# Performance work log

Hardware: AMD Instinct MI355X
Metric: run time of the kernel (lower is better)

The kernel has to match this reference:

```python
import jax, jax.numpy as jnp
import numpy as np

B, S = 1, 2048
D = 4096          # hidden_size
H, HK, DH = 32, 8, 128  # num_heads, num_kv_heads, head_dim
THETA = 10000.0


def setup_inputs() -> dict:
    key = jax.random.key(0)
    k0, k1, k2, k3, k4 = jax.random.split(key, 5)
    std = 0.02
    return {
        "position_ids": jnp.broadcast_to(jnp.arange(S, dtype=jnp.int32), (B, S)),
        "hidden_states": jax.random.normal(k0, (B, S, D), jnp.float32),
        "Wq": (jax.random.normal(k1, (D, H * DH), jnp.float32) * std),
        "Wk": (jax.random.normal(k2, (D, HK * DH), jnp.float32) * std),
        "Wv": (jax.random.normal(k3, (D, HK * DH), jnp.float32) * std),
        "Wo": (jax.random.normal(k4, (H * DH, D), jnp.float32) * std),
    }


def _rope(x, pos):
    """Neox-style rotary embedding over the full head_dim. x: [B,S,h,DH]."""
    half = DH // 2
    inv_freq = 1.0 / (THETA ** (jnp.arange(half, dtype=jnp.float32) * 2.0 / DH))
    ang = pos[..., None].astype(jnp.float32) * inv_freq          # [B,S,half]
    cos = jnp.cos(ang)[:, :, None, :]
    sin = jnp.sin(ang)[:, :, None, :]
    x1, x2 = x[..., :half], x[..., half:]
    return jnp.concatenate([x1 * cos - x2 * sin, x2 * cos + x1 * sin], axis=-1)


def reference(position_ids, hidden_states, Wq, Wk, Wv, Wo):
    q = (hidden_states @ Wq).reshape(B, S, H, DH)
    k = (hidden_states @ Wk).reshape(B, S, HK, DH)
    v = (hidden_states @ Wv).reshape(B, S, HK, DH)
    q = _rope(q, position_ids)
    k = _rope(k, position_ids)

    G = H // HK  # query heads per kv head (GQA)
    qg = q.reshape(B, S, HK, G, DH)
    scale = jnp.float32(DH) ** -0.5
    scores = jnp.einsum('bqhgd,bkhd->bhgqk', qg, k) * scale      # [B,HK,G,S,S]
    causal = jnp.tril(jnp.ones((S, S), dtype=bool))
    scores = jnp.where(causal, scores, jnp.finfo(scores.dtype).min)
    p = jax.nn.softmax(scores, axis=-1)
    out = jnp.einsum('bhgqk,bkhd->bqhgd', p, v).reshape(B, S, H * DH)
    return out @ Wo
```

## Files before the change

kernel.cpp:

```cpp
#include <hip/hip_runtime.h>

typedef unsigned short u16;
typedef short bf16x8 __attribute__((ext_vector_type(8)));
typedef float f32x4 __attribute__((ext_vector_type(4)));

#define GLB __attribute__((address_space(1)))
#define LDSAS __attribute__((address_space(3)))

constexpr int S = 2048, D = 4096, NH = 32, NHK = 8, DHD = 128;
constexpr int NQKV = 6144;

__device__ __forceinline__ u16 f2b(float f) {
    union { float f; unsigned u; } v; v.f = f;
    return (u16)((v.u + 0x7fffu + ((v.u >> 16) & 1u)) >> 16);
}
__device__ __forceinline__ float b2f(u16 b) {
    union { unsigned u; float f; } v; v.u = ((unsigned)b) << 16;
    return v.f;
}
__device__ __forceinline__ void gload16(const void* g, void* l) {
    __builtin_amdgcn_global_load_lds((const GLB unsigned int*)g,
                                     (LDSAS unsigned int*)l, 16, 0, 0);
}
#if __has_builtin(__builtin_amdgcn_exp2f)
__device__ __forceinline__ float exp2fast(float x) { return __builtin_amdgcn_exp2f(x); }
#else
__device__ __forceinline__ float exp2fast(float x) { return __expf(0.6931471805599453f * x); }
#endif

__device__ __forceinline__ void sincos_big(float ang, float* sn, float* cs) {
#if __has_builtin(__builtin_amdgcn_sinf) && __has_builtin(__builtin_amdgcn_cosf)
    float rev = ang * 0.15915494309189535f;
    rev = rev - floorf(rev);
    *sn = __builtin_amdgcn_sinf(rev);
    *cs = __builtin_amdgcn_cosf(rev);
#else
    *sn = sinf(ang);
    *cs = cosf(ang);
#endif
}

__global__ __launch_bounds__(256) void cvt_x(const float* __restrict__ in,
                                             u16* __restrict__ out, int n8) {
    int i = blockIdx.x * 256 + threadIdx.x;
    if (i >= n8) return;
    const float4* p = (const float4*)in + (size_t)i * 2;
    float4 a = p[0], b = p[1];
    uint4 o;
    o.x = f2b(a.x) | ((unsigned)f2b(a.y) << 16);
    o.y = f2b(a.z) | ((unsigned)f2b(a.w) << 16);
    o.z = f2b(b.x) | ((unsigned)f2b(b.y) << 16);
    o.w = f2b(b.z) | ((unsigned)f2b(b.w) << 16);
    *(uint4*)(out + (size_t)i * 8) = o;
}

__global__ __launch_bounds__(256) void tconv(const float* __restrict__ in,
                                             u16* __restrict__ out, int R, int C) {
    __shared__ float t[64][65];
    int r0 = blockIdx.y * 64, c0 = blockIdx.x * 64;
    int tx = threadIdx.x & 63, ty = threadIdx.x >> 6;
#pragma unroll
    for (int i = 0; i < 64; i += 4)
        t[ty + i][tx] = in[(size_t)(r0 + ty + i) * C + c0 + tx];
    __syncthreads();
#pragma unroll
    for (int i = 0; i < 64; i += 4)
        out[(size_t)(c0 + ty + i) * R + r0 + tx] = f2b(t[tx][ty + i]);
}

__global__ __launch_bounds__(256) void vtrans(const u16* __restrict__ QKV,
                                              u16* __restrict__ Vt) {
    __shared__ u16 t[64][65];
    int hk = blockIdx.z;
    int s0 = blockIdx.x * 64, d0 = blockIdx.y * 64;
    int tx = threadIdx.x & 63, ty = threadIdx.x >> 6;
#pragma unroll
    for (int i = 0; i < 64; i += 4)
        t[ty + i][tx] = QKV[(size_t)(s0 + ty + i) * NQKV + 5120 + hk * 128 + d0 + tx];
    __syncthreads();
#pragma unroll
    for (int i = 0; i < 64; i += 4)
        Vt[(size_t)hk * (128 * 2048) + (size_t)(d0 + ty + i) * 2048 + s0 + tx] = t[tx][ty + i];
}

template <int NHEADS>
__global__ __launch_bounds__(256) void rope2(u16* __restrict__ T,
                                             const int* __restrict__ pos, float scale) {
    int idx = blockIdx.x * 256 + threadIdx.x;
    int d = idx & 63;
    int h = (idx >> 6) & (NHEADS - 1);
    int s = idx >> (6 + (NHEADS == 32 ? 5 : 3));
    float p = (float)pos[s];
    float inv = __expf(-(float)d * 0.14391156531310576f);
    float ang = p * inv;
    float sn, cs;
    sincos_big(ang, &sn, &cs);
    size_t base = (size_t)s * NQKV + h * 128 + d;
    float x1 = b2f(T[base]), x2 = b2f(T[base + 64]);
    T[base]      = f2b((x1 * cs - x2 * sn) * scale);
    T[base + 64] = f2b((x2 * cs + x1 * sn) * scale);
}

template <bool BF16OUT>
__global__ __launch_bounds__(256) void gemm_bt(const u16* __restrict__ A,
                                               const u16* __restrict__ Bt,
                                               void* __restrict__ Cout,
                                               int N, int K) {
    __shared__ u16 Asm[128 * 32];
    __shared__ u16 Bsm[128 * 32];
    int tid = threadIdx.x;
    int wave = tid >> 6, lane = tid & 63;
    int l15 = lane & 15, l4 = lane >> 4;
    int m0 = blockIdx.y * 128, n0 = blockIdx.x * 128;
    int wm = wave >> 1, wn = wave & 1;
    f32x4 acc[4][4] = {};
    for (int k0 = 0; k0 < K; k0 += 32) {
        __syncthreads();
#pragma unroll
        for (int it = 0; it < 2; ++it) {
            int ch = wave * 128 + it * 64 + lane;
            int row = ch >> 2, cc = ch & 3;
            gload16(A  + (size_t)(m0 + row) * K + k0 + cc * 8,
                    Asm + (size_t)(wave * 128 + it * 64) * 8);
            gload16(Bt + (size_t)(n0 + row) * K + k0 + cc * 8,
                    Bsm + (size_t)(wave * 128 + it * 64) * 8);
        }
        __syncthreads();
        bf16x8 af[4], bf[4];
#pragma unroll
        for (int i = 0; i < 4; ++i)
            af[i] = *(const bf16x8*)(Asm + (wm * 64 + i * 16 + l15) * 32 + l4 * 8);
#pragma unroll
        for (int j = 0; j < 4; ++j)
            bf[j] = *(const bf16x8*)(Bsm + (wn * 64 + j * 16 + l15) * 32 + l4 * 8);
#pragma unroll
        for (int i = 0; i < 4; ++i)
#pragma unroll
            for (int j = 0; j < 4; ++j)
                acc[i][j] = __builtin_amdgcn_mfma_f32_16x16x32_bf16(af[i], bf[j], acc[i][j], 0, 0, 0);
    }
#pragma unroll
    for (int i = 0; i < 4; ++i)
#pragma unroll
        for (int j = 0; j < 4; ++j) {
            int col  = n0 + wn * 64 + j * 16 + l15;
            int rowb = m0 + wm * 64 + i * 16 + l4 * 4;
#pragma unroll
            for (int r = 0; r < 4; ++r) {
                if (BF16OUT)
                    ((u16*)Cout)[(size_t)(rowb + r) * N + col] = f2b(acc[i][j][r]);
                else
                    ((float*)Cout)[(size_t)(rowb + r) * N + col] = acc[i][j][r];
            }
        }
}

__global__ __launch_bounds__(256) void attn3(const u16* __restrict__ QKV,
                                             const u16* __restrict__ Vt,
                                             u16* __restrict__ O) {
    __shared__ u16 Ksm[2][64 * 128];
    __shared__ u16 Vsm[2][128 * 64];
    __shared__ u16 Psm[4][16 * 64];
    const int orig = blockIdx.x;
    const int swz = (orig & 7) * 64 + (orig >> 3);
    const int h = swz >> 4, p = swz & 15;
    const int hk = h >> 2;
    const int tid = threadIdx.x, wave = tid >> 6, lane = tid & 63;
    const int l15 = lane & 15, l4 = lane >> 4;
    const u16* Qp = QKV + h * 128;
    const u16* Kp = QKV + 4096 + hk * 128;
    const u16* Vp = Vt + (size_t)hk * (128 * 2048);

    auto stage = [&](int kb, int b) {
#pragma unroll
        for (int it = 0; it < 4; ++it) {
            int L = it * 256 + tid;
            int krow = L >> 4, kslot = L & 15;
            int kcs = (kslot & 8) | ((kslot ^ krow) & 7);
            gload16(Kp + (size_t)(kb * 64 + krow) * NQKV + kcs * 8, &Ksm[b][L * 8]);
            int vrow = L >> 3, vslot = L & 7;
            int vcs = (vslot ^ vrow) & 7;
            gload16(Vp + (size_t)vrow * 2048 + kb * 64 + vcs * 8, &Vsm[b][L * 8]);
        }
    };

#pragma unroll 1
    for (int pass = 0; pass < 2; ++pass) {
        const int qt = pass ? p : 31 - p;
        const int qr0 = qt * 64 + wave * 16;
        const int nkb = qt + 1;

        bf16x8 qf[4];
        {
            const u16* qrow = Qp + (size_t)(qr0 + l15) * NQKV;
#pragma unroll
            for (int c = 0; c < 4; ++c)
                qf[c] = *(const bf16x8*)(qrow + c * 32 + l4 * 8);
        }
        float mrow[4], lsum[4];
#pragma unroll
        for (int r = 0; r < 4; ++r) { mrow[r] = -1e30f; lsum[r] = 0.f; }
        f32x4 o[8] = {};

        stage(0, 0);
#pragma unroll 1
        for (int kb = 0; kb < nkb; ++kb) {
            const int cur = kb & 1;
            if (kb + 1 < nkb) {
                stage(kb + 1, cur ^ 1);
                asm volatile("s_waitcnt vmcnt(8)" ::: "memory");
            } else {
                asm volatile("s_waitcnt vmcnt(0)" ::: "memory");
            }
            __builtin_amdgcn_s_barrier();

            if (kb * 64 <= qr0 + 15) {
                const u16* Kb_ = Ksm[cur];
                const u16* Vb_ = Vsm[cur];
                const bool diag = (kb * 64 + 63 > qr0);
                f32x4 sc[4] = {};
#pragma unroll
                for (int f = 0; f < 4; ++f) {
                    const int kv = f * 16 + l15;
#pragma unroll
                    for (int c = 0; c < 4; ++c) {
                        int cd = c * 4 + l4;
                        int cpos = (cd & 8) | ((cd ^ kv) & 7);
                        bf16x8 kf = *(const bf16x8*)(Kb_ + kv * 128 + cpos * 8);
                        sc[f] = __builtin_amdgcn_mfma_f32_16x16x32_bf16(qf[c], kf, sc[f], 0, 0, 0);
                    }
                }
                if (diag) {
#pragma unroll
                    for (int f = 0; f < 4; ++f) {
                        int col = kb * 64 + f * 16 + l15;
#pragma unroll
                        for (int r = 0; r < 4; ++r) {
                            int row = qr0 + l4 * 4 + r;
                            if (col > row) sc[f][r] = -1e30f;
                        }
                    }
                }
                float bm[4];
#pragma unroll
                for (int r = 0; r < 4; ++r)
                    bm[r] = fmaxf(fmaxf(sc[0][r], sc[1][r]), fmaxf(sc[2][r], sc[3][r]));
#pragma unroll
                for (int msk = 1; msk < 16; msk <<= 1)
#pragma unroll
                    for (int r = 0; r < 4; ++r) bm[r] = fmaxf(bm[r], __shfl_xor(bm[r], msk));

                bool need = false;
#pragma unroll
                for (int r = 0; r < 4; ++r) need = need || (bm[r] > mrow[r] + 8.0f);
                if (__any((int)need)) {
                    float al[4];
#pragma unroll
                    for (int r = 0; r < 4; ++r) {
                        float mn = fmaxf(mrow[r], bm[r]);
                        al[r] = exp2fast(mrow[r] - mn);
                        mrow[r] = mn;
                        lsum[r] *= al[r];
                    }
#pragma unroll
                    for (int n = 0; n < 8; ++n)
#pragma unroll
                        for (int r = 0; r < 4; ++r) o[n][r] *= al[r];
                }
                float rs[4] = {0.f, 0.f, 0.f, 0.f};
#pragma unroll
                for (int f = 0; f < 4; ++f) {
#pragma unroll
                    for (int r = 0; r < 4; ++r) {
                        float pw = exp2fast(sc[f][r] - mrow[r]);
                        rs[r] += pw;
                        int q = l4 * 4 + r;
                        int kvc = f * 2 + (l15 >> 3);
                        int slot = (kvc ^ q) & 7;
                        Psm[wave][q * 64 + slot * 8 + (l15 & 7)] = f2b(pw);
                    }
                }
#pragma unroll
                for (int msk = 1; msk < 16; msk <<= 1)
#pragma unroll
                    for (int r = 0; r < 4; ++r) rs[r] += __shfl_xor(rs[r], msk);
#pragma unroll
                for (int r = 0; r < 4; ++r) lsum[r] += rs[r];

                asm volatile("s_waitcnt lgkmcnt(0)" ::: "memory");
                bf16x8 pf[2];
#pragma unroll
                for (int c = 0; c < 2; ++c) {
                    int chc = c * 4 + l4;
                    int slot = (chc ^ l15) & 7;
                    pf[c] = *(const bf16x8*)(&Psm[wave][l15 * 64 + slot * 8]);
                }
#pragma unroll
                for (int n = 0; n < 8; ++n) {
                    int d = n * 16 + l15;
                    bf16x8 vf[2];
#pragma unroll
                    for (int c = 0; c < 2; ++c) {
                        int ch = c * 4 + l4;
                        int slot = (ch ^ d) & 7;
                        vf[c] = *(const bf16x8*)(Vb_ + d * 64 + slot * 8);
                    }
#pragma unroll
                    for (int c = 0; c < 2; ++c)
                        o[n] = __builtin_amdgcn_mfma_f32_16x16x32_bf16(pf[c], vf[c], o[n], 0, 0, 0);
                }
            }
            asm volatile("s_waitcnt lgkmcnt(0)" ::: "memory");
            __builtin_amdgcn_s_barrier();
        }

        float inv[4];
#pragma unroll
        for (int r = 0; r < 4; ++r) inv[r] = 1.0f / lsum[r];
#pragma unroll
        for (int n = 0; n < 8; ++n)
#pragma unroll
            for (int r = 0; r < 4; ++r) {
                int row = qr0 + l4 * 4 + r;
                O[(size_t)row * 4096 + h * 128 + n * 16 + l15] = f2b(o[n][r] * inv[r]);
            }
    }
}

extern "C" void kernel_launch(void* const* d_in, const int* in_sizes, int n_in,
                              void* d_out, int out_size, void* d_ws, size_t ws_size,
                              hipStream_t stream) {
    const int*   pos = (const int*)d_in[0];
    const float* X   = (const float*)d_in[1];
    const float* Wq  = (const float*)d_in[2];
    const float* Wk  = (const float*)d_in[3];
    const float* Wv  = (const float*)d_in[4];
    const float* Wo  = (const float*)d_in[5];
    float* out = (float*)d_out;

    char* w = (char*)d_ws;
    u16* Xb    = (u16*)(w + 0);
    u16* Wqkvt = (u16*)(w + 16777216);
    u16* Wot   = (u16*)(w + 67108864);
    u16* QKV   = (u16*)(w + 100663296);
    u16* Vtb   = (u16*)(w + 125829120);
    u16* Ob    = (u16*)(w + 130023424);

    const float SC2 = 0.08838834764831845f * 1.4426950408889634f;

    cvt_x<<<4096, 256, 0, stream>>>(X, Xb, S * D / 8);
    tconv<<<dim3(64, 64), 256, 0, stream>>>(Wq, Wqkvt, 4096, 4096);
    tconv<<<dim3(16, 64), 256, 0, stream>>>(Wk, Wqkvt + (size_t)4096 * 4096, 4096, 1024);
    tconv<<<dim3(16, 64), 256, 0, stream>>>(Wv, Wqkvt + (size_t)5120 * 4096, 4096, 1024);
    tconv<<<dim3(64, 64), 256, 0, stream>>>(Wo, Wot, 4096, 4096);

    gemm_bt<true><<<dim3(48, 16), 256, 0, stream>>>(Xb, Wqkvt, QKV, NQKV, 4096);

    rope2<32><<<16384, 256, 0, stream>>>(QKV, pos, SC2);
    rope2<8><<<4096, 256, 0, stream>>>(QKV + 4096, pos, 1.0f);

    vtrans<<<dim3(32, 2, 8), 256, 0, stream>>>(QKV, Vtb);

    attn3<<<512, 256, 0, stream>>>(QKV, Vtb, Ob);

    gemm_bt<false><<<dim3(32, 16), 256, 0, stream>>>(Ob, Wot, out, 4096, 4096);
}
```

Measured before the change: 405.7 us.

## Rewrite GEMM with double-buffered LDS, XOR swizzle, 128x256 tiles and XCD remap

Replaces the single-buffered 128x128 GEMM with a 512-thread 128x256-tile kernel that prefetches the next K=64 slice into a second LDS buffer while computing the current one. LDS columns are XOR-swizzled to avoid bank conflicts, and block indices are remapped across the 8 XCDs so neighbouring tiles share L2. MFMA priority hints are added. The cost is much higher LDS use per block (96KB) and fewer blocks, which may limit occupancy and the number of waves in flight.

```diff
diff --git a/kernel.cpp b/kernel.cpp
--- a/kernel.cpp
+++ b/kernel.cpp
@@ -102,42 +102,78 @@
 }
 
 template <bool BF16OUT>
-__global__ __launch_bounds__(256) void gemm_bt(const u16* __restrict__ A,
-                                               const u16* __restrict__ Bt,
-                                               void* __restrict__ Cout,
-                                               int N, int K) {
-    __shared__ u16 Asm[128 * 32];
-    __shared__ u16 Bsm[128 * 32];
-    int tid = threadIdx.x;
-    int wave = tid >> 6, lane = tid & 63;
-    int l15 = lane & 15, l4 = lane >> 4;
-    int m0 = blockIdx.y * 128, n0 = blockIdx.x * 128;
-    int wm = wave >> 1, wn = wave & 1;
+__global__ __launch_bounds__(512, 2) void gemm8(const u16* __restrict__ A,
+                                                const u16* __restrict__ Bt,
+                                                void* __restrict__ Cout,
+                                                int N, int K, int nbx) {
+    __shared__ u16 Asm[2][128 * 64];
+    __shared__ u16 Bsm[2][256 * 64];
+    const int nwg = gridDim.x;
+    const int cpx = nwg >> 3;
+    const int b = ((int)blockIdx.x & 7) * cpx + ((int)blockIdx.x >> 3);
+    const int by = b / nbx, bx = b - by * nbx;
+    const int m0 = by * 128, n0 = bx * 256;
+    const int tid = threadIdx.x;
+    const int lane = tid & 63;
+    const int wave = tid >> 6;
+    const int l15 = lane & 15, l4 = lane >> 4;
+    const int wm = wave >> 2, wn = wave & 3;
     f32x4 acc[4][4] = {};
-    for (int k0 = 0; k0 < K; k0 += 32) {
-        __syncthreads();
-#pragma unroll
-        for (int it = 0; it < 2; ++it) {
-            int ch = wave * 128 + it * 64 + lane;
-            int row = ch >> 2, cc = ch & 3;
-            gload16(A  + (size_t)(m0 + row) * K + k0 + cc * 8,
-                    Asm + (size_t)(wave * 128 + it * 64) * 8);
-            gload16(Bt + (size_t)(n0 + row) * K + k0 + cc * 8,
-                    Bsm + (size_t)(wave * 128 + it * 64) * 8);
-        }
-        __syncthreads();
-        bf16x8 af[4], bf[4];
-#pragma unroll
-        for (int i = 0; i < 4; ++i)
-            af[i] = *(const bf16x8*)(Asm + (wm * 64 + i * 16 + l15) * 32 + l4 * 8);
-#pragma unroll
-        for (int j = 0; j < 4; ++j)
-            bf[j] = *(const bf16x8*)(Bsm + (wn * 64 + j * 16 + l15) * 32 + l4 * 8);
-#pragma unroll
-        for (int i = 0; i < 4; ++i)
-#pragma unroll
-            for (int j = 0; j < 4; ++j)
-                acc[i][j] = __builtin_amdgcn_mfma_f32_16x16x32_bf16(af[i], bf[j], acc[i][j], 0, 0, 0);
+
+    auto stage = [&](int t, int buf) {
+        const int k0 = t * 64;
+#pragma unroll
+        for (int u = 0; u < 2; ++u) {
+            int s = u * 512 + tid;
+            int row = s >> 3, cs = (s & 7) ^ (row & 7);
+            gload16(A + (size_t)(m0 + row) * K + k0 + cs * 8, &Asm[buf][s * 8]);
+        }
+#pragma unroll
+        for (int u = 0; u < 4; ++u) {
+            int s = u * 512 + tid;
+            int row = s >> 3, cs = (s & 7) ^ (row & 7);
+            gload16(Bt + (size_t)(n0 + row) * K + k0 + cs * 8, &Bsm[buf][s * 8]);
+        }
+    };
+
+    const int NT = K >> 6;
+    stage(0, 0);
+#pragma unroll 1
+    for (int t = 0; t < NT; ++t) {
+        const int c = t & 1;
+        if (t + 1 < NT) {
+            stage(t + 1, c ^ 1);
+            asm volatile("s_waitcnt vmcnt(6)" ::: "memory");
+        } else {
+            asm volatile("s_waitcnt vmcnt(0)" ::: "memory");
+        }
+        __builtin_amdgcn_s_barrier();
+#pragma unroll
+        for (int kk = 0; kk < 2; ++kk) {
+            bf16x8 af[4], bf[4];
+#pragma unroll
+            for (int i = 0; i < 4; ++i) {
+                int row = wm * 64 + i * 16 + l15;
+                int cc = (kk * 4 + l4) ^ (row & 7);
+                af[i] = *(const bf16x8*)(&Asm[c][row * 64 + cc * 8]);
+            }
+#pragma unroll
+            for (int j = 0; j < 4; ++j) {
+                int row = wn * 64 + j * 16 + l15;
+                int cc = (kk * 4 + l4) ^ (row & 7);
+                bf[j] = *(const bf16x8*)(&Bsm[c][row * 64 + cc * 8]);
+            }
+            __builtin_amdgcn_s_setprio(1);
+#pragma unroll
+            for (int i = 0; i < 4; ++i)
+#pragma unroll
+                for (int j = 0; j < 4; ++j)
+                    acc[i][j] = __builtin_amdgcn_mfma_f32_16x16x32_bf16(af[i], bf[j], acc[i][j], 0, 0, 0);
+            __builtin_amdgcn_s_setprio(0);
+            if (kk == 0) __builtin_amdgcn_s_barrier();
+        }
+        asm volatile("s_waitcnt lgkmcnt(0)" ::: "memory");
+        __builtin_amdgcn_s_barrier();
     }
 #pragma unroll
     for (int i = 0; i < 4; ++i)
@@ -354,7 +390,7 @@
     tconv<<<dim3(16, 64), 256, 0, stream>>>(Wv, Wqkvt + (size_t)5120 * 4096, 4096, 1024);
     tconv<<<dim3(64, 64), 256, 0, stream>>>(Wo, Wot, 4096, 4096);
 
-    gemm_bt<true><<<dim3(48, 16), 256, 0, stream>>>(Xb, Wqkvt, QKV, NQKV, 4096);
+    gemm8<true><<<384, 512, 0, stream>>>(Xb, Wqkvt, QKV, NQKV, 4096, 24);
 
     rope2<32><<<16384, 256, 0, stream>>>(QKV, pos, SC2);
     rope2<8><<<4096, 256, 0, stream>>>(QKV + 4096, pos, 1.0f);
@@ -363,5 +399,5 @@
 
     attn3<<<512, 256, 0, stream>>>(QKV, Vtb, Ob);
 
-    gemm_bt<false><<<dim3(32, 16), 256, 0, stream>>>(Ob, Wot, out, 4096, 4096);
-}
+    gemm8<false><<<256, 512, 0, stream>>>(Ob, Wot, out, 4096, 4096, 16);
+}
```

After: 430.9 us. +6.2%, slower.

## Widen GEMM K-tile to 64 with XOR-swizzled LDS and XCD-aware block remap

Applied to the files above, without the earlier changes.

The bf16 GEMM kernel now stages 64-wide K slices per iteration instead of 32, which halves the number of barrier pairs per tile. An XOR swizzle on the LDS chunk index is meant to avoid bank conflicts on the fragment reads. A 1D grid with a block-index remap groups consecutive tiles per XCD (blockIdx mod 8) to improve L2 reuse. The cost is doubled LDS use per block, which may lower occupancy, and the loop is still single-buffered.

```diff
diff --git a/kernel.cpp b/kernel.cpp
--- a/kernel.cpp
+++ b/kernel.cpp
@@ -102,42 +102,55 @@
 }
 
 template <bool BF16OUT>
-__global__ __launch_bounds__(256) void gemm_bt(const u16* __restrict__ A,
-                                               const u16* __restrict__ Bt,
-                                               void* __restrict__ Cout,
-                                               int N, int K) {
-    __shared__ u16 Asm[128 * 32];
-    __shared__ u16 Bsm[128 * 32];
-    int tid = threadIdx.x;
-    int wave = tid >> 6, lane = tid & 63;
-    int l15 = lane & 15, l4 = lane >> 4;
-    int m0 = blockIdx.y * 128, n0 = blockIdx.x * 128;
-    int wm = wave >> 1, wn = wave & 1;
+__global__ __launch_bounds__(256) void gemmS(const u16* __restrict__ A,
+                                             const u16* __restrict__ Bt,
+                                             void* __restrict__ Cout,
+                                             int N, int K, int nbx) {
+    __shared__ u16 Asm[128 * 64];
+    __shared__ u16 Bsm[128 * 64];
+    const int cpx = (int)gridDim.x >> 3;
+    const int b = ((int)blockIdx.x & 7) * cpx + ((int)blockIdx.x >> 3);
+    const int by = b / nbx, bx = b - by * nbx;
+    const int m0 = by * 128, n0 = bx * 128;
+    const int tid = threadIdx.x, lane = tid & 63, wave = tid >> 6;
+    const int l15 = lane & 15, l4 = lane >> 4;
+    const int wm = wave >> 1, wn = wave & 1;
     f32x4 acc[4][4] = {};
-    for (int k0 = 0; k0 < K; k0 += 32) {
+
+    for (int k0 = 0; k0 < K; k0 += 64) {
         __syncthreads();
 #pragma unroll
-        for (int it = 0; it < 2; ++it) {
-            int ch = wave * 128 + it * 64 + lane;
-            int row = ch >> 2, cc = ch & 3;
-            gload16(A  + (size_t)(m0 + row) * K + k0 + cc * 8,
-                    Asm + (size_t)(wave * 128 + it * 64) * 8);
-            gload16(Bt + (size_t)(n0 + row) * K + k0 + cc * 8,
-                    Bsm + (size_t)(wave * 128 + it * 64) * 8);
+        for (int u = 0; u < 4; ++u) {
+            int s = u * 256 + tid;
+            int row = s >> 3, cs = (s & 7) ^ (row & 7);
+            gload16(A  + (size_t)(m0 + row) * K + k0 + cs * 8, Asm + s * 8);
+            gload16(Bt + (size_t)(n0 + row) * K + k0 + cs * 8, Bsm + s * 8);
         }
         __syncthreads();
-        bf16x8 af[4], bf[4];
+        bf16x8 af[4][2], bf[4][2];
 #pragma unroll
         for (int i = 0; i < 4; ++i)
-            af[i] = *(const bf16x8*)(Asm + (wm * 64 + i * 16 + l15) * 32 + l4 * 8);
+#pragma unroll
+            for (int kk = 0; kk < 2; ++kk) {
+                int row = wm * 64 + i * 16 + l15;
+                int cc = (kk * 4 + l4) ^ (row & 7);
+                af[i][kk] = *(const bf16x8*)(Asm + row * 64 + cc * 8);
+            }
 #pragma unroll
         for (int j = 0; j < 4; ++j)
-            bf[j] = *(const bf16x8*)(Bsm + (wn * 64 + j * 16 + l15) * 32 + l4 * 8);
+#pragma unroll
+            for (int kk = 0; kk < 2; ++kk) {
+                int row = wn * 64 + j * 16 + l15;
+                int cc = (kk * 4 + l4) ^ (row & 7);
+                bf[j][kk] = *(const bf16x8*)(Bsm + row * 64 + cc * 8);
+            }
 #pragma unroll
         for (int i = 0; i < 4; ++i)
 #pragma unroll
             for (int j = 0; j < 4; ++j)
-                acc[i][j] = __builtin_amdgcn_mfma_f32_16x16x32_bf16(af[i], bf[j], acc[i][j], 0, 0, 0);
+#pragma unroll
+                for (int kk = 0; kk < 2; ++kk)
+                    acc[i][j] = __builtin_amdgcn_mfma_f32_16x16x32_bf16(af[i][kk], bf[j][kk], acc[i][j], 0, 0, 0);
     }
 #pragma unroll
     for (int i = 0; i < 4; ++i)
@@ -354,7 +367,7 @@
     tconv<<<dim3(16, 64), 256, 0, stream>>>(Wv, Wqkvt + (size_t)5120 * 4096, 4096, 1024);
     tconv<<<dim3(64, 64), 256, 0, stream>>>(Wo, Wot, 4096, 4096);
 
-    gemm_bt<true><<<dim3(48, 16), 256, 0, stream>>>(Xb, Wqkvt, QKV, NQKV, 4096);
+    gemmS<true><<<768, 256, 0, stream>>>(Xb, Wqkvt, QKV, NQKV, 4096, 48);
 
     rope2<32><<<16384, 256, 0, stream>>>(QKV, pos, SC2);
     rope2<8><<<4096, 256, 0, stream>>>(QKV + 4096, pos, 1.0f);
@@ -363,5 +376,5 @@
 
     attn3<<<512, 256, 0, stream>>>(QKV, Vtb, Ob);
 
-    gemm_bt<false><<<dim3(32, 16), 256, 0, stream>>>(Ob, Wot, out, 4096, 4096);
-}
+    gemmS<false><<<512, 256, 0, stream>>>(Ob, Wot, out, 4096, 4096, 32);
+}
```

New measurement: 368.0 us. 1.1x faster.
